# Optimization experiments

Measured on AMD Instinct MI355X. Metric: run time of the kernel, lower is better.

The kernel has to match this reference:

```python
import jax, jax.numpy as jnp
import numpy as np

K = 16  # matches init kwarg k


def setup_inputs() -> dict:
    key = jax.random.key(0)
    point_cloud = jax.random.normal(key, (4, 64, 4096), dtype=jnp.float32)
    return {"point_cloud": point_cloud}


def reference(point_cloud):
    B, dims, N = point_cloud.shape
    xt = jnp.transpose(point_cloud, (0, 2, 1))  # (B, N, dims)
    # pairwise euclidean distances (cdist, p=2)
    sq = jnp.sum(xt * xt, axis=-1)  # (B, N)
    d2 = sq[:, :, None] + sq[:, None, :] - 2.0 * jnp.einsum('bnd,bmd->bnm', xt, xt)
    dist = jnp.sqrt(jnp.maximum(d2, 0.0))  # (B, N, N)
    # k+1 smallest distances; drop self (first) neighbor
    _, idx_o = jax.lax.top_k(-dist, K + 1)  # (B, N, K+1)
    idx = idx_o[:, :, 1:]  # (B, N, K)
    # gather neighbor features: neighbors[b,d,n,j] = point_cloud[b,d,idx[b,n,j]]
    neighbors = jax.vmap(lambda pc, i: pc[:, i])(point_cloud, idx)  # (B, dims, N, K)
    central = point_cloud[:, :, :, None]  # (B, dims, N, 1)
    edge_feature = jnp.concatenate(
        [jnp.broadcast_to(central, (B, dims, N, K)), neighbors - central], axis=1
    )  # (B, 2*dims, N, K)
    return edge_feature, idx.reshape(B, -1)
```

## Files before the change

kernel.cpp:

```cpp
#include <hip/hip_runtime.h>


#define BATCH 4
#define DIMS 64
#define NPTS 4096
#define KNN 16
#define NCHUNK 32
#define CHLEN 128
#define GSZ 8
#define RN (BATCH * NPTS)
#define MLANES 8
#define MCH (NCHUNK / MLANES)

typedef unsigned long long u64;
typedef unsigned int u32;

__device__ __forceinline__ double sentinel() {
    return __longlong_as_double(0x7FEFFFFFFFFFFFFFLL);
}

__global__ __launch_bounds__(256) void ef_sq_kernel(const float* __restrict__ pc,
                                                    float* __restrict__ sq) {
    int gid = blockIdx.x * 256 + threadIdx.x;
    int b = gid >> 12;
    int n = gid & (NPTS - 1);
    const float* p = pc + (size_t)b * DIMS * NPTS + n;
    float r[8];
#pragma unroll
    for (int j = 0; j < 8; ++j) {
        float v = p[(size_t)j * NPTS];
        r[j] = __fmul_rn(v, v);
    }
#pragma unroll
    for (int i = 8; i < DIMS; i += 8) {
#pragma unroll
        for (int j = 0; j < 8; ++j) {
            float v = p[(size_t)(i + j) * NPTS];
            r[j] = __fadd_rn(r[j], __fmul_rn(v, v));
        }
    }
    float t01 = __fadd_rn(r[0], r[1]);
    float t23 = __fadd_rn(r[2], r[3]);
    float t45 = __fadd_rn(r[4], r[5]);
    float t67 = __fadd_rn(r[6], r[7]);
    sq[gid] = __fadd_rn(__fadd_rn(t01, t23), __fadd_rn(t45, t67));
}

__global__ __launch_bounds__(256) void ef_transpose(const float* __restrict__ pc,
                                                    float* __restrict__ pcT) {
    __shared__ float smT[DIMS][65];
    int tid = threadIdx.x;
    int m0 = blockIdx.x * 64;
    int b = blockIdx.y;
    const float* pcb = pc + (size_t)b * DIMS * NPTS;
#pragma unroll
    for (int i = 0; i < 16; ++i) {
        int idx = i * 256 + tid;
        int d = idx >> 6;
        int m = idx & 63;
        smT[d][m] = pcb[(size_t)d * NPTS + m0 + m];
    }
    __syncthreads();
#pragma unroll
    for (int i = 0; i < 16; ++i) {
        int idx = i * 256 + tid;
        int m = idx >> 6;
        int d = idx & 63;
        pcT[((size_t)b * NPTS + m0 + m) * DIMS + d] = smT[d][m];
    }
}

__global__ __launch_bounds__(256, 3) void ef_knn_partial(const float* __restrict__ pc,
                                                         const float* __restrict__ sq,
                                                         u64* __restrict__ pKey) {
    __shared__ float tile[DIMS][CHLEN];
    __shared__ float tileSq[CHLEN];
    int tid = threadIdx.x;
    int r = blockIdx.x * 256 + tid;
    int c = blockIdx.y;
    int b = (blockIdx.x * 256) >> 12;
    int n = r & (NPTS - 1);
    int m0 = c * CHLEN;
    const float* pcb = pc + (size_t)b * DIMS * NPTS;

    float xr[DIMS];
#pragma unroll
    for (int d = 0; d < DIMS; ++d) xr[d] = pcb[(size_t)d * NPTS + n];
#pragma unroll
    for (int d = 0; d < DIMS; ++d) asm volatile("" : "+v"(xr[d]));
    float sqn = sq[r];

#pragma unroll
    for (int i = 0; i < 8; ++i) {
        int idx = tid + i * 256;
        int d = idx >> 5;
        int mq = idx & 31;
        float4 v = *(const float4*)(pcb + (size_t)d * NPTS + m0 + mq * 4);
        *(float4*)&tile[d][mq * 4] = v;
    }
    if (tid < CHLEN / 4)
        *(float4*)&tileSq[tid * 4] =
            *(const float4*)(sq + (size_t)b * NPTS + m0 + tid * 4);
    __syncthreads();

    double key[KNN];
#pragma unroll
    for (int j = 0; j < KNN; ++j) key[j] = sentinel();

#define CE(arr, i, jj) { double lo_ = fmin(arr[i], arr[jj]); double hi_ = fmax(arr[i], arr[jj]); arr[i] = lo_; arr[jj] = hi_; }

    for (int g = 0; g < CHLEN; g += GSZ) {
        float acc[GSZ];
#pragma unroll
        for (int j = 0; j < GSZ; ++j) acc[j] = 0.f;
#pragma unroll
        for (int d = 0; d < DIMS; ++d) {
            float xv = xr[d];
            float4 lo = *(const float4*)&tile[d][g];
            float4 hi = *(const float4*)&tile[d][g + 4];
            acc[0] = fmaf(xv, lo.x, acc[0]);
            acc[1] = fmaf(xv, lo.y, acc[1]);
            acc[2] = fmaf(xv, lo.z, acc[2]);
            acc[3] = fmaf(xv, lo.w, acc[3]);
            acc[4] = fmaf(xv, hi.x, acc[4]);
            acc[5] = fmaf(xv, hi.y, acc[5]);
            acc[6] = fmaf(xv, hi.z, acc[6]);
            acc[7] = fmaf(xv, hi.w, acc[7]);
        }
        float4 sq_lo = *(const float4*)&tileSq[g];
        float4 sq_hi = *(const float4*)&tileSq[g + 4];
        float sqv[GSZ] = {sq_lo.x, sq_lo.y, sq_lo.z, sq_lo.w,
                          sq_hi.x, sq_hi.y, sq_hi.z, sq_hi.w};
        double s[GSZ];
#pragma unroll
        for (int j = 0; j < GSZ; ++j) {
            int m = m0 + g + j;
            float t1 = __fadd_rn(sqn, sqv[j]);
            float d2 = __fsub_rn(t1, __fmul_rn(2.0f, acc[j]));
            float dist = __fsqrt_rn(fmaxf(d2, 0.f));
            u64 cu = ((u64)__float_as_uint(dist) << 32) | (u64)(u32)m;
            double cand = __longlong_as_double((long long)cu);
            s[j] = (m == n) ? sentinel() : cand;
        }
        CE(s, 0, 1) CE(s, 2, 3) CE(s, 4, 5) CE(s, 6, 7)
        CE(s, 0, 2) CE(s, 1, 3) CE(s, 4, 6) CE(s, 5, 7)
        CE(s, 1, 2) CE(s, 5, 6)
        CE(s, 0, 4) CE(s, 1, 5) CE(s, 2, 6) CE(s, 3, 7)
        CE(s, 2, 4) CE(s, 3, 5)
        CE(s, 1, 2) CE(s, 3, 4) CE(s, 5, 6)
#pragma unroll
        for (int j = 8; j < 16; ++j) key[j] = fmin(key[j], s[15 - j]);
#pragma unroll
        for (int st = 8; st >= 1; st >>= 1) {
#pragma unroll
            for (int j = 0; j < KNN; ++j) {
                if ((j & st) == 0) {
                    double a = key[j], d = key[j | st];
                    key[j] = fmin(a, d);
                    key[j | st] = fmax(a, d);
                }
            }
        }
    }
#undef CE

    u64* dst = pKey + ((size_t)c * RN + r) * KNN;
#pragma unroll
    for (int j = 0; j < KNN; ++j) dst[j] = (u64)__double_as_longlong(key[j]);
}

__global__ __launch_bounds__(256) void ef_knn_merge(const u64* __restrict__ pKey,
                                                    float* __restrict__ outIdxF) {
    int t = blockIdx.x * 256 + threadIdx.x;
    int r = t >> 3;
    int s = t & 7;
    double key[KNN];
    {
        const u64* src = pKey + ((size_t)(s * MCH) * RN + r) * KNN;
#pragma unroll
        for (int j = 0; j < KNN; ++j)
            key[j] = __longlong_as_double((long long)src[j]);
    }
    for (int ci = 1; ci < MCH; ++ci) {
        const u64* src = pKey + ((size_t)(s * MCH + ci) * RN + r) * KNN;
        double v[KNN];
#pragma unroll
        for (int j = 0; j < KNN; ++j)
            v[j] = __longlong_as_double((long long)src[j]);
#pragma unroll
        for (int j = 0; j < KNN; ++j) key[j] = fmin(key[j], v[KNN - 1 - j]);
#pragma unroll
        for (int st = 8; st >= 1; st >>= 1) {
#pragma unroll
            for (int j = 0; j < KNN; ++j) {
                if ((j & st) == 0) {
                    double a = key[j], d = key[j | st];
                    key[j] = fmin(a, d);
                    key[j | st] = fmax(a, d);
                }
            }
        }
    }
#pragma unroll
    for (int mask = 1; mask <= 4; mask <<= 1) {
        double oth[KNN];
#pragma unroll
        for (int j = 0; j < KNN; ++j) oth[j] = __shfl_xor(key[j], mask, 64);
#pragma unroll
        for (int j = 0; j < KNN; ++j) key[j] = fmin(key[j], oth[KNN - 1 - j]);
#pragma unroll
        for (int st = 8; st >= 1; st >>= 1) {
#pragma unroll
            for (int j = 0; j < KNN; ++j) {
                if ((j & st) == 0) {
                    double a = key[j], d = key[j | st];
                    key[j] = fmin(a, d);
                    key[j | st] = fmax(a, d);
                }
            }
        }
    }
    if (s == 0) {
        float* dstf = outIdxF + (size_t)r * KNN;
#pragma unroll
        for (int j = 0; j < KNN; ++j)
            dstf[j] = (float)(u32)((u64)__double_as_longlong(key[j]) & 0xFFFFFFFFu);
    }
}

__global__ __launch_bounds__(256) void ef_edge_kernelT(const float* __restrict__ pcT,
                                                       const float* __restrict__ idxF,
                                                       float* __restrict__ out) {
    int gid = blockIdx.x * 256 + threadIdx.x;
    int k = gid & 15;
    int n = (gid >> 4) & (NPTS - 1);
    int b = gid >> 16;
    int m = (int)idxF[gid];
    const float* crow = pcT + ((size_t)(b << 12) + n) * DIMS;
    const float* nrow = pcT + ((size_t)(b << 12) + m) * DIMS;
    float* ob = out + (size_t)b * 2 * DIMS * NPTS * KNN + (size_t)n * KNN + k;
#pragma unroll
    for (int q = 0; q < DIMS / 4; ++q) {
        float4 c4 = *(const float4*)(crow + q * 4);
        float4 a4 = *(const float4*)(nrow + q * 4);
        ob[(size_t)(4 * q + 0) * (NPTS * KNN)] = c4.x;
        ob[(size_t)(4 * q + 1) * (NPTS * KNN)] = c4.y;
        ob[(size_t)(4 * q + 2) * (NPTS * KNN)] = c4.z;
        ob[(size_t)(4 * q + 3) * (NPTS * KNN)] = c4.w;
        ob[(size_t)(DIMS + 4 * q + 0) * (NPTS * KNN)] = a4.x - c4.x;
        ob[(size_t)(DIMS + 4 * q + 1) * (NPTS * KNN)] = a4.y - c4.y;
        ob[(size_t)(DIMS + 4 * q + 2) * (NPTS * KNN)] = a4.z - c4.z;
        ob[(size_t)(DIMS + 4 * q + 3) * (NPTS * KNN)] = a4.w - c4.w;
    }
}

__global__ __launch_bounds__(256) void ef_edge_kernel(const float* __restrict__ pc,
                                                      const float* __restrict__ idxF,
                                                      float* __restrict__ out) {
    int gid = blockIdx.x * 256 + threadIdx.x;
    int b = gid >> 16;
    int nk = gid & 65535;
    int n = nk >> 4;
    int m = (int)idxF[gid];
    const float* pcb = pc + (size_t)b * DIMS * NPTS;
    float* ob = out + (size_t)b * 2 * DIMS * NPTS * KNN;
#pragma unroll
    for (int d = 0; d < DIMS; ++d) {
        float cv = pcb[(size_t)d * NPTS + n];
        float nv = pcb[(size_t)d * NPTS + m];
        ob[(size_t)d * (NPTS * KNN) + nk] = cv;
        ob[(size_t)(DIMS + d) * (NPTS * KNN) + nk] = nv - cv;
    }
}

extern "C" void kernel_launch(void* const* d_in, const int* in_sizes, int n_in,
                              void* d_out, int out_size, void* d_ws, size_t ws_size,
                              hipStream_t stream) {
    const float* pc = (const float*)d_in[0];
    float* out = (float*)d_out;

    u64* pKey = (u64*)d_out;
    float* sq = out + 16777216;
    float* outIdxF = out + (size_t)BATCH * 2 * DIMS * NPTS * KNN;
    float* pcT = (float*)d_ws;
    bool useT = ws_size >= (size_t)BATCH * NPTS * DIMS * sizeof(float);

    ef_sq_kernel<<<(BATCH * NPTS) / 256, 256, 0, stream>>>(pc, sq);
    if (useT)
        ef_transpose<<<dim3(NPTS / 64, BATCH), 256, 0, stream>>>(pc, pcT);
    ef_knn_partial<<<dim3(RN / 256, NCHUNK), 256, 0, stream>>>(pc, sq, pKey);
    ef_knn_merge<<<(RN * MLANES) / 256, 256, 0, stream>>>(pKey, outIdxF);
    if (useT)
        ef_edge_kernelT<<<(BATCH * NPTS * KNN) / 256, 256, 0, stream>>>(pcT, outIdxF, out);
    else
        ef_edge_kernel<<<(BATCH * NPTS * KNN) / 256, 256, 0, stream>>>(pc, outIdxF, out);
}
```

Before: 314.0 us.

## Fuse squared-norm into transpose kernel and split edge kernel across dim halves

```diff
diff --git a/kernel.cpp b/kernel.cpp
--- a/kernel.cpp
+++ b/kernel.cpp
@@ -47,7 +47,8 @@
 }
 
 __global__ __launch_bounds__(256) void ef_transpose(const float* __restrict__ pc,
-                                                    float* __restrict__ pcT) {
+                                                    float* __restrict__ pcT,
+                                                    float* __restrict__ sq) {
     __shared__ float smT[DIMS][65];
     int tid = threadIdx.x;
     int m0 = blockIdx.x * 64;
@@ -61,6 +62,29 @@
         smT[d][m] = pcb[(size_t)d * NPTS + m0 + m];
     }
     __syncthreads();
+    if (tid < 64) {
+        int m = tid;
+        float r[8];
+#pragma unroll
+        for (int j = 0; j < 8; ++j) {
+            float v = smT[j][m];
+            r[j] = __fmul_rn(v, v);
+        }
+#pragma unroll
+        for (int i = 8; i < DIMS; i += 8) {
+#pragma unroll
+            for (int j = 0; j < 8; ++j) {
+                float v = smT[i + j][m];
+                r[j] = __fadd_rn(r[j], __fmul_rn(v, v));
+            }
+        }
+        float t01 = __fadd_rn(r[0], r[1]);
+        float t23 = __fadd_rn(r[2], r[3]);
+        float t45 = __fadd_rn(r[4], r[5]);
+        float t67 = __fadd_rn(r[6], r[7]);
+        sq[b * NPTS + m0 + m] =
+            __fadd_rn(__fadd_rn(t01, t23), __fadd_rn(t45, t67));
+    }
 #pragma unroll
     for (int i = 0; i < 16; ++i) {
         int idx = i * 256 + tid;
@@ -231,26 +255,31 @@
 __global__ __launch_bounds__(256) void ef_edge_kernelT(const float* __restrict__ pcT,
                                                        const float* __restrict__ idxF,
                                                        float* __restrict__ out) {
-    int gid = blockIdx.x * 256 + threadIdx.x;
-    int k = gid & 15;
-    int n = (gid >> 4) & (NPTS - 1);
-    int b = gid >> 16;
-    int m = (int)idxF[gid];
-    const float* crow = pcT + ((size_t)(b << 12) + n) * DIMS;
-    const float* nrow = pcT + ((size_t)(b << 12) + m) * DIMS;
-    float* ob = out + (size_t)b * 2 * DIMS * NPTS * KNN + (size_t)n * KNN + k;
-#pragma unroll
-    for (int q = 0; q < DIMS / 4; ++q) {
-        float4 c4 = *(const float4*)(crow + q * 4);
-        float4 a4 = *(const float4*)(nrow + q * 4);
-        ob[(size_t)(4 * q + 0) * (NPTS * KNN)] = c4.x;
-        ob[(size_t)(4 * q + 1) * (NPTS * KNN)] = c4.y;
-        ob[(size_t)(4 * q + 2) * (NPTS * KNN)] = c4.z;
-        ob[(size_t)(4 * q + 3) * (NPTS * KNN)] = c4.w;
-        ob[(size_t)(DIMS + 4 * q + 0) * (NPTS * KNN)] = a4.x - c4.x;
-        ob[(size_t)(DIMS + 4 * q + 1) * (NPTS * KNN)] = a4.y - c4.y;
-        ob[(size_t)(DIMS + 4 * q + 2) * (NPTS * KNN)] = a4.z - c4.z;
-        ob[(size_t)(DIMS + 4 * q + 3) * (NPTS * KNN)] = a4.w - c4.w;
+    int t = blockIdx.x * 256 + threadIdx.x;
+    int k = t & 15;
+    int n = (t >> 4) & (NPTS - 1);
+    int dh = (t >> 16) & 1;
+    int b = t >> 17;
+    int m = (int)idxF[(((size_t)b << 12) + n) * KNN + k];
+    const float* crow = pcT + (((size_t)b << 12) + n) * DIMS + dh * 32;
+    const float* nrow = pcT + (((size_t)b << 12) + m) * DIMS + dh * 32;
+    float4 c[8], a[8];
+#pragma unroll
+    for (int q = 0; q < 8; ++q) c[q] = ((const float4*)crow)[q];
+#pragma unroll
+    for (int q = 0; q < 8; ++q) a[q] = ((const float4*)nrow)[q];
+    float* ob = out + ((size_t)b * 2 * DIMS + dh * 32) * (NPTS * KNN)
+                    + (size_t)n * KNN + k;
+#pragma unroll
+    for (int q = 0; q < 8; ++q) {
+        ob[(size_t)(4 * q + 0) * (NPTS * KNN)] = c[q].x;
+        ob[(size_t)(4 * q + 1) * (NPTS * KNN)] = c[q].y;
+        ob[(size_t)(4 * q + 2) * (NPTS * KNN)] = c[q].z;
+        ob[(size_t)(4 * q + 3) * (NPTS * KNN)] = c[q].w;
+        ob[(size_t)(DIMS + 4 * q + 0) * (NPTS * KNN)] = a[q].x - c[q].x;
+        ob[(size_t)(DIMS + 4 * q + 1) * (NPTS * KNN)] = a[q].y - c[q].y;
+        ob[(size_t)(DIMS + 4 * q + 2) * (NPTS * KNN)] = a[q].z - c[q].z;
+        ob[(size_t)(DIMS + 4 * q + 3) * (NPTS * KNN)] = a[q].w - c[q].w;
     }
 }
 
@@ -285,13 +314,15 @@
     float* pcT = (float*)d_ws;
     bool useT = ws_size >= (size_t)BATCH * NPTS * DIMS * sizeof(float);
 
-    ef_sq_kernel<<<(BATCH * NPTS) / 256, 256, 0, stream>>>(pc, sq);
-    if (useT)
-        ef_transpose<<<dim3(NPTS / 64, BATCH), 256, 0, stream>>>(pc, pcT);
+    if (useT) {
+        ef_transpose<<<dim3(NPTS / 64, BATCH), 256, 0, stream>>>(pc, pcT, sq);
+    } else {
+        ef_sq_kernel<<<(BATCH * NPTS) / 256, 256, 0, stream>>>(pc, sq);
+    }
     ef_knn_partial<<<dim3(RN / 256, NCHUNK), 256, 0, stream>>>(pc, sq, pKey);
     ef_knn_merge<<<(RN * MLANES) / 256, 256, 0, stream>>>(pKey, outIdxF);
     if (useT)
-        ef_edge_kernelT<<<(BATCH * NPTS * KNN) / 256, 256, 0, stream>>>(pcT, outIdxF, out);
+        ef_edge_kernelT<<<(BATCH * NPTS * KNN * 2) / 256, 256, 0, stream>>>(pcT, outIdxF, out);
     else
         ef_edge_kernel<<<(BATCH * NPTS * KNN) / 256, 256, 0, stream>>>(pc, outIdxF, out);
 }
```

After: 314.1 us. Within noise of the previous version (+0.0%).
